# Optimization experiments

Measured on AMD Instinct MI355X. Metric: run time of the kernel, lower is better.

The kernel has to match this reference:

```python
import jax, jax.numpy as jnp
import numpy as np

C = 256          # in_channels == out_channels
K = 4            # number of parallel depthwise kernels
RED = 4          # SE reduction
KS = 3           # kernel size


def setup_inputs() -> dict:
    key = jax.random.key(0)
    ks = jax.random.split(key, 6)
    B, H, W = 32, 64, 64
    x = jax.random.normal(ks[0], (B, C, H, W), dtype=jnp.float32)
    # K depthwise kernels; per-conv torch weight shape = (C, 1, 3, 3)
    conv_w = jax.random.normal(ks[1], (K, C, 1, KS, KS), dtype=jnp.float32) * 0.1
    fc1_w = jax.random.normal(ks[2], (C // RED, C), dtype=jnp.float32) * (1.0 / np.sqrt(C))
    fc1_b = jnp.zeros((C // RED,), dtype=jnp.float32)
    fc2_w = jax.random.normal(ks[3], (K, C // RED), dtype=jnp.float32) * (1.0 / np.sqrt(C // RED))
    fc2_b = jnp.zeros((K,), dtype=jnp.float32)
    return {"x": x, "conv_w": conv_w, "fc1_w": fc1_w, "fc1_b": fc1_b,
            "fc2_w": fc2_w, "fc2_b": fc2_b}


def reference(x, conv_w, fc1_w, fc1_b, fc2_w, fc2_b):
    B, c, H, W = x.shape
    # --- attention branch: GAP -> fc -> relu -> fc -> softmax over K ---
    g = jnp.mean(x, axis=(2, 3))                       # [B, C]
    h = jax.nn.relu(g @ fc1_w.T + fc1_b)               # [B, C//r]
    attn = jax.nn.softmax(h @ fc2_w.T + fc2_b, axis=1) # [B, K]
    # --- all K depthwise convs as ONE grouped conv with K*C output channels ---
    # group i (input channel i) produces output channels [i*K:(i+1)*K],
    # so arrange weights as (C, K, 1, ks, ks) -> (C*K, 1, ks, ks)
    w_all = jnp.transpose(conv_w, (1, 0, 2, 3, 4)).reshape(c * K, 1, KS, KS)
    out = jax.lax.conv_general_dilated(
        x, w_all, window_strides=(1, 1), padding=[(1, 1), (1, 1)],
        feature_group_count=c,
        dimension_numbers=("NCHW", "OIHW", "NCHW"))    # [B, C*K, H, W]
    out = out.reshape(B, c, K, H, W)
    # attention-weighted sum over the K kernels
    return jnp.einsum("bckhw,bk->bchw", out, attn)
```

## Files before the change

kernel.cpp:

```cpp
#include <hip/hip_runtime.h>

#define CH 256
#define KK 4
#define HW 64
#define PLANE 4096
#define TS 67

typedef float fx4 __attribute__((ext_vector_type(4)));

__global__ __launch_bounds__(256) void gap_kernel(const float* __restrict__ x,
                                                  float* __restrict__ g) {
    int plane = blockIdx.x;
    const float4* p = (const float4*)(x + (size_t)plane * PLANE);
    float sum = 0.f;
    #pragma unroll
    for (int k = 0; k < 4; ++k) {
        float4 v = p[threadIdx.x + k * 256];
        sum += (v.x + v.y) + (v.z + v.w);
    }
    for (int off = 32; off > 0; off >>= 1)
        sum += __shfl_down(sum, off);
    __shared__ float ws[4];
    int lane = threadIdx.x & 63;
    int wid  = threadIdx.x >> 6;
    if (lane == 0) ws[wid] = sum;
    __syncthreads();
    if (threadIdx.x == 0)
        g[plane] = (ws[0] + ws[1] + ws[2] + ws[3]) * (1.f / PLANE);
}

__global__ __launch_bounds__(64) void attn_kernel(const float* __restrict__ g,
                            const float* __restrict__ fc1_w, const float* __restrict__ fc1_b,
                            const float* __restrict__ fc2_w, const float* __restrict__ fc2_b,
                            float* __restrict__ attn) {
    int b = blockIdx.x;
    int t = threadIdx.x;
    __shared__ float gs[CH];
    __shared__ float h[64];
    __shared__ float logit[KK];
    for (int i = t; i < CH; i += 64) gs[i] = g[b * CH + i];
    __syncthreads();
    {
        const float4* wr = (const float4*)(fc1_w + t * CH);
        const float4* gv = (const float4*)gs;
        float a0 = fc1_b[t], a1 = 0.f, a2 = 0.f, a3 = 0.f;
        #pragma unroll 4
        for (int i = 0; i < CH / 4; ++i) {
            float4 w4 = wr[i], g4 = gv[i];
            a0 = fmaf(w4.x, g4.x, a0);
            a1 = fmaf(w4.y, g4.y, a1);
            a2 = fmaf(w4.z, g4.z, a2);
            a3 = fmaf(w4.w, g4.w, a3);
        }
        h[t] = fmaxf((a0 + a1) + (a2 + a3), 0.f);
    }
    __syncthreads();
    if (t < KK) {
        const float4* w2 = (const float4*)(fc2_w + t * 64);
        const float4* hv = (const float4*)h;
        float a0 = fc2_b[t], a1 = 0.f, a2 = 0.f, a3 = 0.f;
        #pragma unroll
        for (int i = 0; i < 16; ++i) {
            float4 w4 = w2[i], h4 = hv[i];
            a0 = fmaf(w4.x, h4.x, a0);
            a1 = fmaf(w4.y, h4.y, a1);
            a2 = fmaf(w4.z, h4.z, a2);
            a3 = fmaf(w4.w, h4.w, a3);
        }
        logit[t] = (a0 + a1) + (a2 + a3);
    }
    __syncthreads();
    if (t == 0) {
        float m = fmaxf(fmaxf(logit[0], logit[1]), fmaxf(logit[2], logit[3]));
        float e[KK];
        float s = 0.f;
        #pragma unroll
        for (int k = 0; k < KK; ++k) { e[k] = __expf(logit[k] - m); s += e[k]; }
        float inv = 1.f / s;
        #pragma unroll
        for (int k = 0; k < KK; ++k) attn[b * KK + k] = e[k] * inv;
    }
}

__global__ __launch_bounds__(256) void dwconv_kernel(const float* __restrict__ x,
                              const float* __restrict__ conv_w,
                              const float* __restrict__ attn, float* __restrict__ out) {
    int plane = blockIdx.x;
    int b = plane >> 8;
    int c = plane & (CH - 1);
    __shared__ float tile[66 * TS];
    int t = threadIdx.x;

    for (int i = t; i < 260; i += 256) {
        int idx;
        if (i < 66)       idx = i;
        else if (i < 132) idx = 65 * TS + (i - 66);
        else if (i < 196) idx = (i - 131) * TS;
        else              idx = (i - 195) * TS + 65;
        tile[idx] = 0.f;
    }

    const float4* xp4 = (const float4*)(x + (size_t)plane * PLANE);
    #pragma unroll
    for (int k = 0; k < 4; ++k) {
        int idx = t + k * 256;
        int y   = idx >> 4;
        int xq  = (idx & 15) << 2;
        float4 v = xp4[idx];
        float* d = &tile[(y + 1) * TS + 1 + xq];
        d[0] = v.x; d[1] = v.y; d[2] = v.z; d[3] = v.w;
    }

    float a0 = attn[b * KK + 0], a1 = attn[b * KK + 1],
          a2 = attn[b * KK + 2], a3 = attn[b * KK + 3];
    float w[9];
    #pragma unroll
    for (int j = 0; j < 9; ++j) {
        w[j] = a0 * conv_w[(0 * CH + c) * 9 + j]
             + a1 * conv_w[(1 * CH + c) * 9 + j]
             + a2 * conv_w[(2 * CH + c) * 9 + j]
             + a3 * conv_w[(3 * CH + c) * 9 + j];
    }
    __syncthreads();

    int y0 = t >> 4;
    int xq = (t & 15) << 2;
    fx4* op4 = (fx4*)(out + (size_t)plane * PLANE);
    #pragma unroll
    for (int gi = 0; gi < 4; ++gi) {
        int y = y0 + gi * 16;
        float s0 = 0.f, s1 = 0.f, s2 = 0.f, s3 = 0.f;
        #pragma unroll
        for (int dy = 0; dy < 3; ++dy) {
            const float* r = &tile[(y + dy) * TS + xq];
            float e0 = r[0], e1 = r[1], e2 = r[2], e3 = r[3], e4 = r[4], e5 = r[5];
            float w0 = w[dy * 3], w1 = w[dy * 3 + 1], w2 = w[dy * 3 + 2];
            s0 = fmaf(e0, w0, fmaf(e1, w1, fmaf(e2, w2, s0)));
            s1 = fmaf(e1, w0, fmaf(e2, w1, fmaf(e3, w2, s1)));
            s2 = fmaf(e2, w0, fmaf(e3, w1, fmaf(e4, w2, s2)));
            s3 = fmaf(e3, w0, fmaf(e4, w1, fmaf(e5, w2, s3)));
        }
        fx4 res = {s0, s1, s2, s3};
        __builtin_nontemporal_store(res, &op4[(y << 4) + (t & 15)]);
    }
}

extern "C" void kernel_launch(void* const* d_in, const int* in_sizes, int n_in,
                              void* d_out, int out_size, void* d_ws, size_t ws_size,
                              hipStream_t stream) {
    const float* x      = (const float*)d_in[0];
    const float* conv_w = (const float*)d_in[1];
    const float* fc1_w  = (const float*)d_in[2];
    const float* fc1_b  = (const float*)d_in[3];
    const float* fc2_w  = (const float*)d_in[4];
    const float* fc2_b  = (const float*)d_in[5];
    float* out = (float*)d_out;

    int B = in_sizes[0] / (CH * HW * HW);

    float* g    = (float*)d_ws;
    float* attn = g + B * CH;

    gap_kernel <<<B * CH, 256, 0, stream>>>(x, g);
    attn_kernel<<<B, 64, 0, stream>>>(g, fc1_w, fc1_b, fc2_w, fc2_b, attn);
    dwconv_kernel<<<B * CH, 256, 0, stream>>>(x, conv_w, attn, out);
}
```

Before: 262.4 us.

## Fuse GAP, attention, and depthwise conv into one cooperative kernel with grid sync

Replaces the three-kernel pipeline with a single cooperative kernel. Each block reduces 16 planes for the global average, waits at a grid-wide sync, recomputes the small attention MLP for its batch, then runs the depthwise conv over the same 16 planes. The goal is to drop two launches and keep x in L2 between the reduction and the conv. In exchange, every block redundantly recomputes the MLP, and the grid of 512 blocks at 2 blocks per CU must be co-resident. If the cooperative launch fails, the code falls back to the old three kernels.

```diff
diff --git a/kernel.cpp b/kernel.cpp
--- a/kernel.cpp
+++ b/kernel.cpp
@@ -1,12 +1,150 @@
 #include <hip/hip_runtime.h>
+#include <hip/hip_cooperative_groups.h>
+
+namespace cg = cooperative_groups;
 
 #define CH 256
 #define KK 4
-#define HW 64
 #define PLANE 4096
 #define TS 67
+#define PPB 16
 
 typedef float fx4 __attribute__((ext_vector_type(4)));
+
+__global__ __launch_bounds__(256, 2) void fused_kernel(
+    const float* __restrict__ x, const float* __restrict__ conv_w,
+    const float* __restrict__ fc1_w, const float* __restrict__ fc1_b,
+    const float* __restrict__ fc2_w, const float* __restrict__ fc2_b,
+    float* __restrict__ g, float* __restrict__ out)
+{
+    __shared__ float tile[66 * TS];
+    __shared__ float gs[CH];
+    __shared__ float hbuf[64];
+    __shared__ float logits[KK];
+    __shared__ float attn_s[KK];
+
+    int t    = threadIdx.x;
+    int lane = t & 63, wid = t >> 6;
+    int p0   = blockIdx.x * PPB;
+
+    for (int j = 0; j < 4; ++j) {
+        int plane = p0 + wid * 4 + j;
+        const float4* p = (const float4*)(x + (size_t)plane * PLANE);
+        float sum = 0.f;
+        #pragma unroll
+        for (int k = 0; k < 16; ++k) {
+            float4 v = p[lane + k * 64];
+            sum += (v.x + v.y) + (v.z + v.w);
+        }
+        for (int off = 32; off > 0; off >>= 1)
+            sum += __shfl_down(sum, off);
+        if (lane == 0) g[plane] = sum * (1.f / PLANE);
+    }
+
+    cg::this_grid().sync();
+
+    int b = p0 >> 8;
+    gs[t] = g[b * CH + t];
+    __syncthreads();
+    if (t < 64) {
+        const float4* wr = (const float4*)(fc1_w + t * CH);
+        const float4* gv = (const float4*)gs;
+        float a0 = fc1_b[t], a1 = 0.f, a2 = 0.f, a3 = 0.f;
+        #pragma unroll 4
+        for (int i = 0; i < CH / 4; ++i) {
+            float4 w4 = wr[i], g4 = gv[i];
+            a0 = fmaf(w4.x, g4.x, a0);
+            a1 = fmaf(w4.y, g4.y, a1);
+            a2 = fmaf(w4.z, g4.z, a2);
+            a3 = fmaf(w4.w, g4.w, a3);
+        }
+        hbuf[t] = fmaxf((a0 + a1) + (a2 + a3), 0.f);
+    }
+    __syncthreads();
+    if (t < KK) {
+        const float4* w2 = (const float4*)(fc2_w + t * 64);
+        const float4* hv = (const float4*)hbuf;
+        float a0 = fc2_b[t], a1 = 0.f, a2 = 0.f, a3 = 0.f;
+        #pragma unroll
+        for (int i = 0; i < 16; ++i) {
+            float4 w4 = w2[i], h4 = hv[i];
+            a0 = fmaf(w4.x, h4.x, a0);
+            a1 = fmaf(w4.y, h4.y, a1);
+            a2 = fmaf(w4.z, h4.z, a2);
+            a3 = fmaf(w4.w, h4.w, a3);
+        }
+        logits[t] = (a0 + a1) + (a2 + a3);
+    }
+    __syncthreads();
+    if (t == 0) {
+        float m = fmaxf(fmaxf(logits[0], logits[1]), fmaxf(logits[2], logits[3]));
+        float e0 = __expf(logits[0] - m), e1 = __expf(logits[1] - m),
+              e2 = __expf(logits[2] - m), e3 = __expf(logits[3] - m);
+        float inv = 1.f / (e0 + e1 + e2 + e3);
+        attn_s[0] = e0 * inv; attn_s[1] = e1 * inv;
+        attn_s[2] = e2 * inv; attn_s[3] = e3 * inv;
+    }
+
+    for (int i = t; i < 260; i += 256) {
+        int idx;
+        if (i < 66)       idx = i;
+        else if (i < 132) idx = 65 * TS + (i - 66);
+        else if (i < 196) idx = (i - 131) * TS;
+        else              idx = (i - 195) * TS + 65;
+        tile[idx] = 0.f;
+    }
+    __syncthreads();
+
+    float a0 = attn_s[0], a1 = attn_s[1], a2 = attn_s[2], a3 = attn_s[3];
+
+    for (int j = 0; j < PPB; ++j) {
+        int plane = p0 + j;
+        int c = plane & (CH - 1);
+
+        float w[9];
+        #pragma unroll
+        for (int jj = 0; jj < 9; ++jj) {
+            w[jj] = a0 * conv_w[(0 * CH + c) * 9 + jj]
+                  + a1 * conv_w[(1 * CH + c) * 9 + jj]
+                  + a2 * conv_w[(2 * CH + c) * 9 + jj]
+                  + a3 * conv_w[(3 * CH + c) * 9 + jj];
+        }
+
+        const float4* xp4 = (const float4*)(x + (size_t)plane * PLANE);
+        #pragma unroll
+        for (int k = 0; k < 4; ++k) {
+            int idx = t + k * 256;
+            int y   = idx >> 4;
+            int xq  = (idx & 15) << 2;
+            float4 v = xp4[idx];
+            float* d = &tile[(y + 1) * TS + 1 + xq];
+            d[0] = v.x; d[1] = v.y; d[2] = v.z; d[3] = v.w;
+        }
+        __syncthreads();
+
+        int y0 = t >> 4;
+        int xq = (t & 15) << 2;
+        fx4* op4 = (fx4*)(out + (size_t)plane * PLANE);
+        #pragma unroll
+        for (int gi = 0; gi < 4; ++gi) {
+            int y = y0 + gi * 16;
+            float s0 = 0.f, s1 = 0.f, s2 = 0.f, s3 = 0.f;
+            #pragma unroll
+            for (int dy = 0; dy < 3; ++dy) {
+                const float* r = &tile[(y + dy) * TS + xq];
+                float e0 = r[0], e1 = r[1], e2 = r[2], e3 = r[3], e4 = r[4], e5 = r[5];
+                float w0 = w[dy * 3], w1 = w[dy * 3 + 1], w2 = w[dy * 3 + 2];
+                s0 = fmaf(e0, w0, fmaf(e1, w1, fmaf(e2, w2, s0)));
+                s1 = fmaf(e1, w0, fmaf(e2, w1, fmaf(e3, w2, s1)));
+                s2 = fmaf(e2, w0, fmaf(e3, w1, fmaf(e4, w2, s2)));
+                s3 = fmaf(e3, w0, fmaf(e4, w1, fmaf(e5, w2, s3)));
+            }
+            fx4 res = {s0, s1, s2, s3};
+            __builtin_nontemporal_store(res, &op4[(y << 4) + (t & 15)]);
+        }
+        __syncthreads();
+    }
+}
 
 __global__ __launch_bounds__(256) void gap_kernel(const float* __restrict__ x,
                                                   float* __restrict__ g) {
@@ -154,14 +292,20 @@
     const float* fc1_b  = (const float*)d_in[3];
     const float* fc2_w  = (const float*)d_in[4];
     const float* fc2_b  = (const float*)d_in[5];
-    float* out = (float*)d_out;
-
-    int B = in_sizes[0] / (CH * HW * HW);
-
+    float* out  = (float*)d_out;
     float* g    = (float*)d_ws;
-    float* attn = g + B * CH;
-
-    gap_kernel <<<B * CH, 256, 0, stream>>>(x, g);
-    attn_kernel<<<B, 64, 0, stream>>>(g, fc1_w, fc1_b, fc2_w, fc2_b, attn);
-    dwconv_kernel<<<B * CH, 256, 0, stream>>>(x, conv_w, attn, out);
-}
+    float* attn = g + 32 * CH;
+
+    int B    = in_sizes[0] / (CH * PLANE);
+    int nblk = (B * CH) / PPB;
+
+    void* args[] = {(void*)&x, (void*)&conv_w, (void*)&fc1_w, (void*)&fc1_b,
+                    (void*)&fc2_w, (void*)&fc2_b, (void*)&g, (void*)&out};
+    hipError_t e = hipLaunchCooperativeKernel((const void*)fused_kernel, dim3(nblk),
+                                              dim3(256), args, 0, stream);
+    if (e != hipSuccess) {
+        gap_kernel <<<B * CH, 256, 0, stream>>>(x, g);
+        attn_kernel<<<B, 64, 0, stream>>>(g, fc1_w, fc1_b, fc2_w, fc2_b, attn);
+        dwconv_kernel<<<B * CH, 256, 0, stream>>>(x, conv_w, attn, out);
+    }
+}
```

After: 343.8 us. 1.31x slower.
